# Optimization experiments

Hardware: AMD Instinct MI355X
Metric: run time of the kernel (lower is better)

## Reference

```python
import jax, jax.numpy as jnp
import numpy as np

EPS = 1e-5

def layernorm(x, w, b):
    m = jnp.mean(x, axis=-1, keepdims=True)
    v = jnp.var(x, axis=-1, keepdims=True)
    return (x - m) * jax.lax.rsqrt(v + EPS) * w + b

def setup_inputs() -> dict:
    key = jax.random.key(0)
    ks = jax.random.split(key, 20)
    B, N, D, H, C = 4, 2048, 512, 8, 3
    HID = int(D * 4.0 * (2.0 / 3.0))  # SwiGLU hidden = 1365
    g = lambda k, shape, s: (jax.random.normal(k, shape, jnp.float32) * s)
    return {
        "x": g(ks[0], (B, N, D), 1.0),
        "coords": jax.random.uniform(ks[1], (B, N, C), jnp.float32),
        "ln1_w": jnp.ones((D,), jnp.float32),
        "ln1_b": jnp.zeros((D,), jnp.float32),
        "ln2_w": jnp.ones((D,), jnp.float32),
        "ln2_b": jnp.zeros((D,), jnp.float32),
        "Wqkv": g(ks[2], (D, 3 * D), D ** -0.5),
        "bqkv": jnp.zeros((3 * D,), jnp.float32),
        "Wo": g(ks[3], (D, D), D ** -0.5),
        "bo": jnp.zeros((D,), jnp.float32),
        "Wc": g(ks[4], (C, H), 0.1),
        "bc": jnp.zeros((H,), jnp.float32),
        "W1": g(ks[5], (D, HID), D ** -0.5),
        "b1": jnp.zeros((HID,), jnp.float32),
        "W2": g(ks[6], (D, HID), D ** -0.5),
        "b2": jnp.zeros((HID,), jnp.float32),
        "W3": g(ks[7], (HID, D), HID ** -0.5),
        "b3": jnp.zeros((D,), jnp.float32),
    }

def reference(x, coords, ln1_w, ln1_b, ln2_w, ln2_b, Wqkv, bqkv, Wo, bo,
              Wc, bc, W1, b1, W2, b2, W3, b3):
    B, N, D = x.shape
    H = bc.shape[0]
    dh = D // H
    # --- coord-aware patch attention (pre-norm) ---
    h = layernorm(x, ln1_w, ln1_b)
    qkv = h @ Wqkv + bqkv                                # [B,N,3D]
    q, k, v = jnp.split(qkv, 3, axis=-1)
    to_heads = lambda t: t.reshape(B, N, H, dh).transpose(0, 2, 1, 3)  # [B,H,N,dh]
    q, k, v = to_heads(q), to_heads(k), to_heads(v)
    scores = jnp.einsum("bhnd,bhmd->bhnm", q, k) / np.sqrt(dh)
    rel = coords[:, :, None, :] - coords[:, None, :, :]  # [B,N,N,C]
    bias = jnp.einsum("bnmc,ch->bhnm", rel, Wc) + bc[None, :, None, None]
    attn = jax.nn.softmax(scores + bias, axis=-1)
    o = jnp.einsum("bhnm,bhmd->bhnd", attn, v)
    o = o.transpose(0, 2, 1, 3).reshape(B, N, D)
    x = x + (o @ Wo + bo)                                # residual 1
    # --- SwiGLU FFN (pre-norm) ---
    h2 = layernorm(x, ln2_w, ln2_b)
    ff = jax.nn.silu(h2 @ W1 + b1) * (h2 @ W2 + b2)
    x = x + (ff @ W3 + b3)                               # residual 2
    return x
```

## Files before the change

kernel.cpp:

```cpp
#include <hip/hip_runtime.h>
#include <hip/hip_bf16.h>
#include <math.h>

#define B_   4
#define N_   2048
#define D_   512
#define H_   8
#define DH_  64
#define C_   3
#define HID_ 1365
#define HIDP 1408
#define ROWS_ (B_*N_)
#define TD_  (3*D_)

typedef __attribute__((ext_vector_type(8))) short short8;
typedef __attribute__((ext_vector_type(4))) float floatx4;
typedef __attribute__((ext_vector_type(2))) unsigned uint2v;

#define MFMA16(a,b,c) __builtin_amdgcn_mfma_f32_16x16x32_bf16(a,b,c,0,0,0)

typedef __attribute__((address_space(3))) unsigned lds_u32;
typedef __attribute__((address_space(1))) unsigned glb_u32;

__device__ __forceinline__ short sh(float v){
  union { __hip_bfloat16 b; short s; } u;
  u.b = __float2bfloat16(v);
  return u.s;
}

__device__ __forceinline__ unsigned pk2(float a, float b){
  union { short s[2]; unsigned u; } z;
  z.s[0] = sh(a); z.s[1] = sh(b);
  return z.u;
}

__device__ __forceinline__ int swz(int col, int row){
  return (col & ~63) | (col & 7) | ((((col >> 3) & 7) ^ (row & 7)) << 3);
}

template<int ROWS, int PITCH>
__device__ __forceinline__ void stageG(short* __restrict__ lds,
    const short* __restrict__ g, int ldg, int t){
  const int LPR = PITCH/8;
  const int RPI = 64/LPR;
  const int PW  = (ROWS/RPI)/4;
  int lane = t & 63, w = t >> 6;
  #pragma unroll
  for (int i = 0; i < PW; ++i){
    int r0  = (w*PW + i)*RPI;
    int row = r0 + lane/LPR;
    const short* ga = g + (size_t)row*ldg + (lane % LPR)*8;
    short* la = lds + r0*PITCH;
    __builtin_amdgcn_global_load_lds((const glb_u32*)ga, (lds_u32*)la, 16, 0, 0);
  }
}

__device__ __forceinline__ short8 fragS(const short* __restrict__ lds, int pitch,
    int mbase, int lane, int kk){
  int row  = mbase + (lane & 15);
  int seg  = (kk >> 3) + (lane >> 4);
  int phys = seg ^ (row & 7);
  return *(const short8*)(lds + row*pitch + phys*8);
}

__global__ __launch_bounds__(256) void convT_all(
    const float* __restrict__ Wqkv, const float* __restrict__ Wo,
    const float* __restrict__ W1, const float* __restrict__ W2,
    const float* __restrict__ W3,
    short* __restrict__ Wtqkv, short* __restrict__ Wto,
    short* __restrict__ Wt1, short* __restrict__ Wt2, short* __restrict__ Wt3,
    const float* __restrict__ coords, const float* __restrict__ Wc,
    float* __restrict__ tv,
    const float* __restrict__ x, const float* __restrict__ ln1_w,
    const float* __restrict__ ln1_b, short* __restrict__ h){
  int id = blockIdx.x;
  int t = threadIdx.x;
  if (id >= 3392){
    int row = id - 3392;
    size_t base = (size_t)row * D_;
    float v0 = x[base + t];
    float v1 = x[base + t + 256];
    float s  = v0 + v1;
    float s2 = v0*v0 + v1*v1;
    #pragma unroll
    for (int off = 32; off >= 1; off >>= 1){
      s  += __shfl_xor(s,  off, 64);
      s2 += __shfl_xor(s2, off, 64);
    }
    __shared__ float red[8];
    int lane = t & 63, wv = t >> 6;
    if (lane == 0){ red[wv] = s; red[4+wv] = s2; }
    __syncthreads();
    float sum  = red[0]+red[1]+red[2]+red[3];
    float sum2 = red[4]+red[5]+red[6]+red[7];
    float mean = sum * (1.0f/D_);
    float var  = sum2 * (1.0f/D_) - mean*mean;
    float inv  = rsqrtf(fmaxf(var, 0.f) + 1e-5f);
    h[base + swz(t,     row)] = sh((v0-mean)*inv*ln1_w[t]     + ln1_b[t]);
    h[base + swz(t+256, row)] = sh((v1-mean)*inv*ln1_w[t+256] + ln1_b[t+256]);
    return;
  }
  if (id >= 3136){
    int idx = (id - 3136)*256 + t;
    int n = idx & (N_-1);
    int hh = (idx >> 11) & (H_-1);
    int b = idx >> 14;
    float s = 0.f;
    #pragma unroll
    for (int cc = 0; cc < C_; ++cc)
      s += coords[((size_t)(b*N_+n))*C_ + cc] * Wc[cc*H_ + hh];
    tv[idx] = s;
    return;
  }
  __shared__ float tile[32][33];
  const float* in; short* out; int K, NN, Kp, nx;
  if (id < 768)      { in=Wqkv; out=Wtqkv; K=512;  NN=1536; Kp=512;  nx=48; }
  else if (id < 1024){ in=Wo;   out=Wto;   K=512;  NN=512;  Kp=512;  nx=16; id-=768; }
  else if (id < 1728){ in=W1;   out=Wt1;   K=512;  NN=HID_; Kp=512;  nx=44; id-=1024; }
  else if (id < 2432){ in=W2;   out=Wt2;   K=512;  NN=HID_; Kp=512;  nx=44; id-=1728; }
  else               { in=W3;   out=Wt3;   K=HID_; NN=512;  Kp=HIDP; nx=16; id-=2432; }
  int nt0 = (id % nx)*32, kt0 = (id / nx)*32;
  int r = t >> 5, cc = t & 31;
  #pragma unroll
  for (int i=0;i<4;++i){
    int k = kt0 + i*8 + r, n = nt0 + cc;
    tile[i*8+r][cc] = (k<K && n<NN) ? in[(size_t)k*NN + n] : 0.f;
  }
  __syncthreads();
  #pragma unroll
  for (int i=0;i<4;++i){
    int n = nt0 + i*8 + r, k = kt0 + cc;
    out[(size_t)n*Kp + swz(k, n)] = sh(tile[cc][i*8+r]);
  }
}

__global__ __launch_bounds__(256) void ln_kernel(const float* __restrict__ x,
        const float* __restrict__ w, const float* __restrict__ b,
        short* __restrict__ out){
  int row = blockIdx.x;
  size_t base = (size_t)row * D_;
  int t = threadIdx.x;
  float v0 = x[base + t];
  float v1 = x[base + t + 256];
  float s  = v0 + v1;
  float s2 = v0*v0 + v1*v1;
  #pragma unroll
  for (int off = 32; off >= 1; off >>= 1){
    s  += __shfl_xor(s,  off, 64);
    s2 += __shfl_xor(s2, off, 64);
  }
  __shared__ float red[8];
  int lane = t & 63, wv = t >> 6;
  if (lane == 0){ red[wv] = s; red[4+wv] = s2; }
  __syncthreads();
  float sum  = red[0]+red[1]+red[2]+red[3];
  float sum2 = red[4]+red[5]+red[6]+red[7];
  float mean = sum * (1.0f/D_);
  float var  = sum2 * (1.0f/D_) - mean*mean;
  float inv  = rsqrtf(fmaxf(var, 0.f) + 1e-5f);
  out[base + swz(t,     row)] = sh((v0-mean)*inv*w[t]     + b[t]);
  out[base + swz(t+256, row)] = sh((v1-mean)*inv*w[t+256] + b[t+256]);
}

__global__ __launch_bounds__(256) void qkv_gemm(
    const short* __restrict__ A, const short* __restrict__ Bt,
    const float* __restrict__ bias,
    short* __restrict__ qb, short* __restrict__ kb, short* __restrict__ vbt){
  __shared__ short As[128*64];
  __shared__ short Bs[128*64];
  int t = threadIdx.x;
  int lane = t & 63, w = t >> 6;
  int wr = (w >> 1) * 64, wc = (w & 1) * 64;
  int col0 = blockIdx.x * 128, row0 = blockIdx.y * 128;
  floatx4 acc[4][4];
  #pragma unroll
  for (int mt=0;mt<4;++mt)
    #pragma unroll
    for (int nt=0;nt<4;++nt) acc[mt][nt] = (floatx4){0.f,0.f,0.f,0.f};
  for (int k0 = 0; k0 < D_; k0 += 64){
    __syncthreads();
    stageG<128,64>(As, A  + (size_t)row0*D_ + k0, D_, t);
    stageG<128,64>(Bs, Bt + (size_t)col0*D_ + k0, D_, t);
    __syncthreads();
    #pragma unroll
    for (int kk = 0; kk < 64; kk += 32){
      short8 af[4], bf[4];
      #pragma unroll
      for (int mt=0;mt<4;++mt) af[mt] = fragS(As, 64, wr+mt*16, lane, kk);
      #pragma unroll
      for (int nt=0;nt<4;++nt) bf[nt] = fragS(Bs, 64, wc+nt*16, lane, kk);
      #pragma unroll
      for (int mt=0;mt<4;++mt)
        #pragma unroll
        for (int nt=0;nt<4;++nt)
          acc[mt][nt] = MFMA16(af[mt], bf[nt], acc[mt][nt]);
    }
  }
  int quad = lane >> 4, c = lane & 15;
  #pragma unroll
  for (int mt=0;mt<4;++mt){
    #pragma unroll
    for (int nt=0;nt<4;++nt){
      #pragma unroll
      for (int r=0;r<4;++r){
        int row = row0 + wr + mt*16 + quad*4 + r;
        int col = col0 + wc + nt*16 + c;
        float v = acc[mt][nt][r] + bias[col];
        int bidx = row >> 11, n = row & (N_-1);
        int which = col >> 9, d = col & (D_-1), hh = d >> 6, hd = d & 63;
        short sv = sh(v);
        if (which == 0)
          qb[(((size_t)(bidx*H_ + hh))*N_ + n)*DH_ + swz(hd, n)] = sv;
        else if (which == 1)
          kb[(((size_t)(bidx*H_ + hh))*N_ + n)*DH_ + swz(hd, n)] = sv;
        else
          vbt[(((size_t)(bidx*H_ + hh))*DH_ + hd)*N_ + swz(n, hd)] = sv;
      }
    }
  }
}

__global__ __launch_bounds__(256) void gemm64(
    const short* __restrict__ A, int lda,
    const short* __restrict__ Bt, int Ktot,
    const float* __restrict__ bias,
    const float* __restrict__ resid, float* __restrict__ outF){
  __shared__ short As[128*64];
  __shared__ short Bs[64*64];
  int t = threadIdx.x, lane = t & 63, w = t >> 6;
  int wr = w * 32;
  int col0 = blockIdx.x * 64, row0 = blockIdx.y * 128;
  floatx4 acc[2][4];
  #pragma unroll
  for (int mt=0;mt<2;++mt)
    #pragma unroll
    for (int nt=0;nt<4;++nt) acc[mt][nt] = (floatx4){0.f,0.f,0.f,0.f};
  for (int k0 = 0; k0 < Ktot; k0 += 64){
    __syncthreads();
    stageG<128,64>(As, A  + (size_t)row0*lda + k0, lda, t);
    stageG<64,64> (Bs, Bt + (size_t)col0*Ktot + k0, Ktot, t);
    __syncthreads();
    #pragma unroll
    for (int kk = 0; kk < 64; kk += 32){
      short8 af[2], bf[4];
      #pragma unroll
      for (int mt=0;mt<2;++mt) af[mt] = fragS(As, 64, wr+mt*16, lane, kk);
      #pragma unroll
      for (int nt=0;nt<4;++nt) bf[nt] = fragS(Bs, 64, nt*16, lane, kk);
      #pragma unroll
      for (int mt=0;mt<2;++mt)
        #pragma unroll
        for (int nt=0;nt<4;++nt)
          acc[mt][nt] = MFMA16(af[mt], bf[nt], acc[mt][nt]);
    }
  }
  int quad = lane >> 4, c = lane & 15;
  #pragma unroll
  for (int mt=0;mt<2;++mt){
    #pragma unroll
    for (int nt=0;nt<4;++nt){
      #pragma unroll
      for (int r=0;r<4;++r){
        int row = row0 + wr + mt*16 + quad*4 + r;
        int col = col0 + nt*16 + c;
        size_t idx = (size_t)row*D_ + col;
        outF[idx] = acc[mt][nt][r] + bias[col] + resid[idx];
      }
    }
  }
}

__global__ __launch_bounds__(256) void gate_gemm(
    const short* __restrict__ A,
    const short* __restrict__ Bt1, const short* __restrict__ Bt2,
    const float* __restrict__ b1, const float* __restrict__ b2,
    short* __restrict__ ff){
  __shared__ short As[128*64];
  __shared__ short B1s[64*64];
  __shared__ short B2s[64*64];
  int t = threadIdx.x, lane = t & 63, w = t >> 6;
  int wr = (w >> 1) * 64, wc = (w & 1) * 32;
  int col0 = blockIdx.x * 64, row0 = blockIdx.y * 128;
  floatx4 a1[4][2], a2[4][2];
  #pragma unroll
  for (int mt=0;mt<4;++mt)
    #pragma unroll
    for (int nt=0;nt<2;++nt){
      a1[mt][nt] = (floatx4){0.f,0.f,0.f,0.f};
      a2[mt][nt] = (floatx4){0.f,0.f,0.f,0.f};
    }
  for (int k0 = 0; k0 < D_; k0 += 64){
    __syncthreads();
    stageG<128,64>(As, A + (size_t)row0*D_ + k0, D_, t);
    stageG<64,64>(B1s, Bt1 + (size_t)col0*D_ + k0, D_, t);
    stageG<64,64>(B2s, Bt2 + (size_t)col0*D_ + k0, D_, t);
    __syncthreads();
    #pragma unroll
    for (int kk = 0; kk < 64; kk += 32){
      short8 af[4], f1[2], f2[2];
      #pragma unroll
      for (int mt=0;mt<4;++mt) af[mt] = fragS(As, 64, wr+mt*16, lane, kk);
      #pragma unroll
      for (int nt=0;nt<2;++nt){
        f1[nt] = fragS(B1s, 64, wc+nt*16, lane, kk);
        f2[nt] = fragS(B2s, 64, wc+nt*16, lane, kk);
      }
      #pragma unroll
      for (int mt=0;mt<4;++mt)
        #pragma unroll
        for (int nt=0;nt<2;++nt){
          a1[mt][nt] = MFMA16(af[mt], f1[nt], a1[mt][nt]);
          a2[mt][nt] = MFMA16(af[mt], f2[nt], a2[mt][nt]);
        }
    }
  }
  int quad = lane >> 4, c = lane & 15;
  #pragma unroll
  for (int mt=0;mt<4;++mt){
    #pragma unroll
    for (int nt=0;nt<2;++nt){
      #pragma unroll
      for (int r=0;r<4;++r){
        int row = row0 + wr + mt*16 + quad*4 + r;
        int col = col0 + wc + nt*16 + c;
        float g1 = a1[mt][nt][r] + (col < HID_ ? b1[col] : 0.f);
        float g2 = a2[mt][nt][r] + (col < HID_ ? b2[col] : 0.f);
        float sig = 1.f / (1.f + __expf(-g1));
        ff[(size_t)row*HIDP + swz(col, row)] = sh(g1*sig*g2);
      }
    }
  }
}

#define EXP2SC 0.18033688011112042f
__global__ __launch_bounds__(256) void attn_mfma(
    const short* __restrict__ qb, const short* __restrict__ kbuf,
    const short* __restrict__ vbt, const float* __restrict__ tv,
    short* __restrict__ o){
  __shared__ short Ks2[2][128*64];
  __shared__ short Vt2[2][64*128];
  __shared__ __align__(16) float tsAll[2048];
  int qt = blockIdx.x, h = blockIdx.y, b = blockIdx.z;
  int bh = b*H_ + h;
  int t = threadIdx.x, lane = t & 63, w = t >> 6;
  int quad = lane >> 4, c = lane & 15;
  const short* Kbase = kbuf + (size_t)bh*N_*DH_;
  const short* Vbase = vbt  + (size_t)bh*DH_*N_;

  #pragma unroll
  for (int i = 0; i < 8; ++i)
    tsAll[i*256 + t] = tv[(size_t)bh*N_ + i*256 + t] * 1.44269504f;
  stageG<128,64>(Ks2[1], qb + ((size_t)bh*N_ + qt*128)*DH_, DH_, t);
  stageG<128,64>(Ks2[0], Kbase, DH_, t);
  stageG<64,128>(Vt2[0], Vbase, N_, t);
  __syncthreads();
  short8 qf[2][2];
  #pragma unroll
  for (int mt=0;mt<2;++mt)
    #pragma unroll
    for (int kh=0;kh<2;++kh)
      qf[mt][kh] = fragS(Ks2[1], 64, w*32 + mt*16, lane, kh*32);
  floatx4 O[2][4];
  float l_i[2] = {0.f, 0.f};
  #pragma unroll
  for (int mt=0;mt<2;++mt)
    #pragma unroll
    for (int nt=0;nt<4;++nt) O[mt][nt] = (floatx4){0.f,0.f,0.f,0.f};
  __syncthreads();

  for (int kt = 0; kt < N_/128; ++kt){
    int cur = kt & 1;
    if (kt + 1 < N_/128){
      stageG<128,64>(Ks2[cur^1], Kbase + (size_t)(kt+1)*128*DH_, DH_, t);
      stageG<64,128>(Vt2[cur^1], Vbase + (kt+1)*128, N_, t);
    }
    const short* Kc  = Ks2[cur];
    const short* Vc  = Vt2[cur];
    const float* tsc = tsAll + kt*128;
    #pragma unroll
    for (int kb4 = 0; kb4 < 4; ++kb4){
      floatx4 St[2][2];
      #pragma unroll
      for (int i=0;i<2;++i){
        St[i][0] = (floatx4){0.f,0.f,0.f,0.f};
        St[i][1] = (floatx4){0.f,0.f,0.f,0.f};
      }
      #pragma unroll
      for (int kh=0;kh<2;++kh){
        short8 kf0 = fragS(Kc, 64, kb4*32,      lane, kh*32);
        short8 kf1 = fragS(Kc, 64, kb4*32 + 16, lane, kh*32);
        #pragma unroll
        for (int mt=0;mt<2;++mt){
          St[0][mt] = MFMA16(kf0, qf[mt][kh], St[0][mt]);
          St[1][mt] = MFMA16(kf1, qf[mt][kh], St[1][mt]);
        }
      }
      floatx4 t0 = *(const floatx4*)&tsc[kb4*32 + quad*4];
      floatx4 t1 = *(const floatx4*)&tsc[kb4*32 + 16 + quad*4];
      short8 pbf[2];
      #pragma unroll
      for (int mt=0;mt<2;++mt){
        float p0[4], p1[4];
        #pragma unroll
        for (int r=0;r<4;++r){
          p0[r] = __builtin_amdgcn_exp2f(fmaf(St[0][mt][r], EXP2SC, -t0[r]));
          p1[r] = __builtin_amdgcn_exp2f(fmaf(St[1][mt][r], EXP2SC, -t1[r]));
        }
        l_i[mt] += (p0[0]+p0[1]) + (p0[2]+p0[3]) + (p1[0]+p1[1]) + (p1[2]+p1[3]);
        unsigned X0 = pk2(p0[0], p0[1]), X1 = pk2(p0[2], p0[3]);
        unsigned Y0 = pk2(p1[0], p1[1]), Y1 = pk2(p1[2], p1[3]);
        auto u0 = __builtin_amdgcn_permlane32_swap(X0, Y0, false, false);
        auto v0 = __builtin_amdgcn_permlane16_swap(u0[0], u0[1], false, false);
        auto u1 = __builtin_amdgcn_permlane32_swap(X1, Y1, false, false);
        auto v1 = __builtin_amdgcn_permlane16_swap(u1[0], u1[1], false, false);
        union { short8 s; unsigned uu[4]; } pb;
        pb.uu[0] = v0[0]; pb.uu[1] = v1[0]; pb.uu[2] = v0[1]; pb.uu[3] = v1[1];
        pbf[mt] = pb.s;
      }
      #pragma unroll
      for (int nt=0;nt<4;++nt){
        short8 vf = fragS(Vc, 128, nt*16, lane, kb4*32);
        #pragma unroll
        for (int mt=0;mt<2;++mt)
          O[mt][nt] = MFMA16(vf, pbf[mt], O[mt][nt]);
      }
    }
    __syncthreads();
  }
  #pragma unroll
  for (int mt=0;mt<2;++mt){
    float l = l_i[mt];
    l += __shfl_xor(l, 16, 64);
    l += __shfl_xor(l, 32, 64);
    float invl = 1.f / l;
    int qrow = qt*128 + w*32 + mt*16 + c;
    size_t rb = ((size_t)b*N_ + qrow)*(size_t)D_;
    #pragma unroll
    for (int nt=0;nt<4;++nt){
      int d0 = h*DH_ + nt*16 + quad*4;
      uint2v pv;
      pv.x = pk2(O[mt][nt][0]*invl, O[mt][nt][1]*invl);
      pv.y = pk2(O[mt][nt][2]*invl, O[mt][nt][3]*invl);
      *(uint2v*)(o + rb + swz(d0, qrow)) = pv;
    }
  }
}

extern "C" void kernel_launch(void* const* d_in, const int* in_sizes, int n_in,
                              void* d_out, int out_size, void* d_ws, size_t ws_size,
                              hipStream_t stream){
  const float* x      = (const float*)d_in[0];
  const float* coords = (const float*)d_in[1];
  const float* ln1_w  = (const float*)d_in[2];
  const float* ln1_b  = (const float*)d_in[3];
  const float* ln2_w  = (const float*)d_in[4];
  const float* ln2_b  = (const float*)d_in[5];
  const float* Wqkv   = (const float*)d_in[6];
  const float* bqkv   = (const float*)d_in[7];
  const float* Wo     = (const float*)d_in[8];
  const float* bo     = (const float*)d_in[9];
  const float* Wc     = (const float*)d_in[10];
  const float* W1     = (const float*)d_in[12];
  const float* b1     = (const float*)d_in[13];
  const float* W2     = (const float*)d_in[14];
  const float* b2     = (const float*)d_in[15];
  const float* W3     = (const float*)d_in[16];
  const float* b3     = (const float*)d_in[17];

  char* ws = (char*)d_ws;
  short* Wtqkv = (short*)(ws);
  short* Wto   = (short*)(ws + 1572864);
  short* Wt1   = (short*)(ws + 2097152);
  short* Wt2   = (short*)(ws + 3538944);
  short* Wt3   = (short*)(ws + 4980736);
  float* tv    = (float*)(ws + 6422528);
  short* h     = (short*)(ws + 6684672);
  short* qb    = (short*)(ws + 15073280);
  short* kb    = (short*)(ws + 23461888);
  short* vbt   = (short*)(ws + 31850496);
  short* o     = h;
  short* h2    = h;
  short* ff    = qb;
  float* x1    = (float*)d_out;

  convT_all<<<dim3(11584), dim3(256), 0, stream>>>(Wqkv, Wo, W1, W2, W3,
      Wtqkv, Wto, Wt1, Wt2, Wt3, coords, Wc, tv, x, ln1_w, ln1_b, h);
  qkv_gemm<<<dim3(12,64), dim3(256), 0, stream>>>(h, Wtqkv, bqkv, qb, kb, vbt);
  attn_mfma<<<dim3(16,8,4), dim3(256), 0, stream>>>(qb, kb, vbt, tv, o);
  gemm64<<<dim3(8,64), dim3(256), 0, stream>>>(o, 512, Wto, 512, bo, x, x1);
  ln_kernel<<<dim3(ROWS_), dim3(256), 0, stream>>>(x1, ln2_w, ln2_b, h2);
  gate_gemm<<<dim3(22,64), dim3(256), 0, stream>>>(h2, Wt1, Wt2, b1, b2, ff);
  gemm64<<<dim3(8,64), dim3(256), 0, stream>>>(ff, HIDP, Wt3, HIDP, b3, x1, x1);
}
```

Baseline: 310.8 us.

## Split attention key blocks across two wave groups with LDS reduction

Doubles the attention workgroup to 8 waves: four query groups times two key halves. Each half handles two of the four 32-key sub-blocks per tile, and partial outputs and row sums are combined through reused LDS before the final write. The log2e scaling of the coordinate bias moves into the precompute kernel, and tile loading uses vectorized loads. This aims to raise occupancy and latency hiding in attention, at the cost of an extra LDS reduction and higher per-block resource demand.

```diff
diff --git a/kernel.cpp b/kernel.cpp
--- a/kernel.cpp
+++ b/kernel.cpp
@@ -38,12 +38,12 @@
   return (col & ~63) | (col & 7) | ((((col >> 3) & 7) ^ (row & 7)) << 3);
 }
 
-template<int ROWS, int PITCH>
+template<int ROWS, int PITCH, int WAVES = 4>
 __device__ __forceinline__ void stageG(short* __restrict__ lds,
     const short* __restrict__ g, int ldg, int t){
   const int LPR = PITCH/8;
   const int RPI = 64/LPR;
-  const int PW  = (ROWS/RPI)/4;
+  const int PW  = (ROWS/RPI)/WAVES;
   int lane = t & 63, w = t >> 6;
   #pragma unroll
   for (int i = 0; i < PW; ++i){
@@ -109,7 +109,7 @@
     #pragma unroll
     for (int cc = 0; cc < C_; ++cc)
       s += coords[((size_t)(b*N_+n))*C_ + cc] * Wc[cc*H_ + hh];
-    tv[idx] = s;
+    tv[idx] = s * 1.44269504f;
     return;
   }
   __shared__ float tile[32][33];
@@ -333,7 +333,7 @@
 }
 
 #define EXP2SC 0.18033688011112042f
-__global__ __launch_bounds__(256) void attn_mfma(
+__global__ __launch_bounds__(512,4) void attn_mfma(
     const short* __restrict__ qb, const short* __restrict__ kbuf,
     const short* __restrict__ vbt, const float* __restrict__ tv,
     short* __restrict__ o){
@@ -343,23 +343,22 @@
   int qt = blockIdx.x, h = blockIdx.y, b = blockIdx.z;
   int bh = b*H_ + h;
   int t = threadIdx.x, lane = t & 63, w = t >> 6;
+  int qg = w & 3, kg = w >> 2;
   int quad = lane >> 4, c = lane & 15;
   const short* Kbase = kbuf + (size_t)bh*N_*DH_;
   const short* Vbase = vbt  + (size_t)bh*DH_*N_;
 
-  #pragma unroll
-  for (int i = 0; i < 8; ++i)
-    tsAll[i*256 + t] = tv[(size_t)bh*N_ + i*256 + t] * 1.44269504f;
-  stageG<128,64>(Ks2[1], qb + ((size_t)bh*N_ + qt*128)*DH_, DH_, t);
-  stageG<128,64>(Ks2[0], Kbase, DH_, t);
-  stageG<64,128>(Vt2[0], Vbase, N_, t);
+  *(floatx4*)&tsAll[t*4] = *(const floatx4*)&tv[(size_t)bh*N_ + t*4];
+  stageG<128,64,8>(Ks2[1], qb + ((size_t)bh*N_ + qt*128)*DH_, DH_, t);
+  stageG<128,64,8>(Ks2[0], Kbase, DH_, t);
+  stageG<64,128,8>(Vt2[0], Vbase, N_, t);
   __syncthreads();
   short8 qf[2][2];
   #pragma unroll
   for (int mt=0;mt<2;++mt)
     #pragma unroll
     for (int kh=0;kh<2;++kh)
-      qf[mt][kh] = fragS(Ks2[1], 64, w*32 + mt*16, lane, kh*32);
+      qf[mt][kh] = fragS(Ks2[1], 64, qg*32 + mt*16, lane, kh*32);
   floatx4 O[2][4];
   float l_i[2] = {0.f, 0.f};
   #pragma unroll
@@ -371,14 +370,15 @@
   for (int kt = 0; kt < N_/128; ++kt){
     int cur = kt & 1;
     if (kt + 1 < N_/128){
-      stageG<128,64>(Ks2[cur^1], Kbase + (size_t)(kt+1)*128*DH_, DH_, t);
-      stageG<64,128>(Vt2[cur^1], Vbase + (kt+1)*128, N_, t);
+      stageG<128,64,8>(Ks2[cur^1], Kbase + (size_t)(kt+1)*128*DH_, DH_, t);
+      stageG<64,128,8>(Vt2[cur^1], Vbase + (kt+1)*128, N_, t);
     }
     const short* Kc  = Ks2[cur];
     const short* Vc  = Vt2[cur];
     const float* tsc = tsAll + kt*128;
     #pragma unroll
-    for (int kb4 = 0; kb4 < 4; ++kb4){
+    for (int kb = 0; kb < 2; ++kb){
+      int kb4 = kg*2 + kb;
       floatx4 St[2][2];
       #pragma unroll
       for (int i=0;i<2;++i){
@@ -427,21 +427,42 @@
     }
     __syncthreads();
   }
-  #pragma unroll
-  for (int mt=0;mt<2;++mt){
-    float l = l_i[mt];
-    l += __shfl_xor(l, 16, 64);
-    l += __shfl_xor(l, 32, 64);
-    float invl = 1.f / l;
-    int qrow = qt*128 + w*32 + mt*16 + c;
-    size_t rb = ((size_t)b*N_ + qrow)*(size_t)D_;
-    #pragma unroll
-    for (int nt=0;nt<4;++nt){
-      int d0 = h*DH_ + nt*16 + quad*4;
-      uint2v pv;
-      pv.x = pk2(O[mt][nt][0]*invl, O[mt][nt][1]*invl);
-      pv.y = pk2(O[mt][nt][2]*invl, O[mt][nt][3]*invl);
-      *(uint2v*)(o + rb + swz(d0, qrow)) = pv;
+  float* Om = (float*)Vt2;
+  float* Lm = (float*)Ks2;
+  if (kg == 1){
+    #pragma unroll
+    for (int mt=0;mt<2;++mt){
+      #pragma unroll
+      for (int nt=0;nt<4;++nt)
+        *(floatx4*)&Om[(((qg*2+mt)*4+nt)*64 + lane)*4] = O[mt][nt];
+      Lm[(qg*2+mt)*64 + lane] = l_i[mt];
+    }
+  }
+  __syncthreads();
+  if (kg == 0){
+    #pragma unroll
+    for (int mt=0;mt<2;++mt){
+      l_i[mt] += Lm[(qg*2+mt)*64 + lane];
+      #pragma unroll
+      for (int nt=0;nt<4;++nt)
+        O[mt][nt] += *(const floatx4*)&Om[(((qg*2+mt)*4+nt)*64 + lane)*4];
+    }
+    #pragma unroll
+    for (int mt=0;mt<2;++mt){
+      float l = l_i[mt];
+      l += __shfl_xor(l, 16, 64);
+      l += __shfl_xor(l, 32, 64);
+      float invl = 1.f / l;
+      int qrow = qt*128 + qg*32 + mt*16 + c;
+      size_t rb = ((size_t)b*N_ + qrow)*(size_t)D_;
+      #pragma unroll
+      for (int nt=0;nt<4;++nt){
+        int d0 = h*DH_ + nt*16 + quad*4;
+        uint2v pv;
+        pv.x = pk2(O[mt][nt][0]*invl, O[mt][nt][1]*invl);
+        pv.y = pk2(O[mt][nt][2]*invl, O[mt][nt][3]*invl);
+        *(uint2v*)(o + rb + swz(d0, qrow)) = pv;
+      }
     }
   }
 }
@@ -486,7 +507,7 @@
   convT_all<<<dim3(11584), dim3(256), 0, stream>>>(Wqkv, Wo, W1, W2, W3,
       Wtqkv, Wto, Wt1, Wt2, Wt3, coords, Wc, tv, x, ln1_w, ln1_b, h);
   qkv_gemm<<<dim3(12,64), dim3(256), 0, stream>>>(h, Wtqkv, bqkv, qb, kb, vbt);
-  attn_mfma<<<dim3(16,8,4), dim3(256), 0, stream>>>(qb, kb, vbt, tv, o);
+  attn_mfma<<<dim3(16,8,4), dim3(512), 0, stream>>>(qb, kb, vbt, tv, o);
   gemm64<<<dim3(8,64), dim3(256), 0, stream>>>(o, 512, Wto, 512, bo, x, x1);
   ln_kernel<<<dim3(ROWS_), dim3(256), 0, stream>>>(x1, ln2_w, ln2_b, h2);
   gate_gemm<<<dim3(22,64), dim3(256), 0, stream>>>(h2, Wt1, Wt2, b1, b2, ff);
```

After: 321.4 us. 3.4% more time.

## Double-buffer gemm64 LDS tiles and vectorize layernorm and bias-table loads

Applied to the files above, without the earlier changes.

gemm64 now keeps two LDS buffers for A and B. The next K-tile is prefetched with global_load_lds while MFMAs run on the current tile, leaving one barrier per iteration and hiding load latency. The two layernorm kernels read x, w and b as float2 and write packed bf16 pairs. The log2e scaling of the coordinate bias table moves into the precompute kernel, so attention loads that table with 16-byte vector loads. The cost is double the LDS in gemm64, which may lower occupancy.

```diff
diff --git a/kernel.cpp b/kernel.cpp
--- a/kernel.cpp
+++ b/kernel.cpp
@@ -38,12 +38,12 @@
   return (col & ~63) | (col & 7) | ((((col >> 3) & 7) ^ (row & 7)) << 3);
 }
 
-template<int ROWS, int PITCH>
+template<int ROWS, int PITCH, int WAVES = 4>
 __device__ __forceinline__ void stageG(short* __restrict__ lds,
     const short* __restrict__ g, int ldg, int t){
   const int LPR = PITCH/8;
   const int RPI = 64/LPR;
-  const int PW  = (ROWS/RPI)/4;
+  const int PW  = (ROWS/RPI)/WAVES;
   int lane = t & 63, w = t >> 6;
   #pragma unroll
   for (int i = 0; i < PW; ++i){
@@ -78,10 +78,9 @@
   if (id >= 3392){
     int row = id - 3392;
     size_t base = (size_t)row * D_;
-    float v0 = x[base + t];
-    float v1 = x[base + t + 256];
-    float s  = v0 + v1;
-    float s2 = v0*v0 + v1*v1;
+    float2 u = *(const float2*)&x[base + 2*t];
+    float s  = u.x + u.y;
+    float s2 = u.x*u.x + u.y*u.y;
     #pragma unroll
     for (int off = 32; off >= 1; off >>= 1){
       s  += __shfl_xor(s,  off, 64);
@@ -96,8 +95,10 @@
     float mean = sum * (1.0f/D_);
     float var  = sum2 * (1.0f/D_) - mean*mean;
     float inv  = rsqrtf(fmaxf(var, 0.f) + 1e-5f);
-    h[base + swz(t,     row)] = sh((v0-mean)*inv*ln1_w[t]     + ln1_b[t]);
-    h[base + swz(t+256, row)] = sh((v1-mean)*inv*ln1_w[t+256] + ln1_b[t+256]);
+    float2 wv2 = *(const float2*)&ln1_w[2*t];
+    float2 bv2 = *(const float2*)&ln1_b[2*t];
+    *(unsigned*)(h + base + swz(2*t, row)) =
+        pk2((u.x-mean)*inv*wv2.x + bv2.x, (u.y-mean)*inv*wv2.y + bv2.y);
     return;
   }
   if (id >= 3136){
@@ -109,7 +110,7 @@
     #pragma unroll
     for (int cc = 0; cc < C_; ++cc)
       s += coords[((size_t)(b*N_+n))*C_ + cc] * Wc[cc*H_ + hh];
-    tv[idx] = s;
+    tv[idx] = s * 1.44269504f;
     return;
   }
   __shared__ float tile[32][33];
@@ -140,10 +141,9 @@
   int row = blockIdx.x;
   size_t base = (size_t)row * D_;
   int t = threadIdx.x;
-  float v0 = x[base + t];
-  float v1 = x[base + t + 256];
-  float s  = v0 + v1;
-  float s2 = v0*v0 + v1*v1;
+  float2 u = *(const float2*)&x[base + 2*t];
+  float s  = u.x + u.y;
+  float s2 = u.x*u.x + u.y*u.y;
   #pragma unroll
   for (int off = 32; off >= 1; off >>= 1){
     s  += __shfl_xor(s,  off, 64);
@@ -158,8 +158,10 @@
   float mean = sum * (1.0f/D_);
   float var  = sum2 * (1.0f/D_) - mean*mean;
   float inv  = rsqrtf(fmaxf(var, 0.f) + 1e-5f);
-  out[base + swz(t,     row)] = sh((v0-mean)*inv*w[t]     + b[t]);
-  out[base + swz(t+256, row)] = sh((v1-mean)*inv*w[t+256] + b[t+256]);
+  float2 wv2 = *(const float2*)&w[2*t];
+  float2 bv2 = *(const float2*)&b[2*t];
+  *(unsigned*)(out + base + swz(2*t, row)) =
+      pk2((u.x-mean)*inv*wv2.x + bv2.x, (u.y-mean)*inv*wv2.y + bv2.y);
 }
 
 __global__ __launch_bounds__(256) void qkv_gemm(
@@ -225,8 +227,8 @@
     const short* __restrict__ Bt, int Ktot,
     const float* __restrict__ bias,
     const float* __restrict__ resid, float* __restrict__ outF){
-  __shared__ short As[128*64];
-  __shared__ short Bs[64*64];
+  __shared__ short As[2][128*64];
+  __shared__ short Bs[2][64*64];
   int t = threadIdx.x, lane = t & 63, w = t >> 6;
   int wr = w * 32;
   int col0 = blockIdx.x * 64, row0 = blockIdx.y * 128;
@@ -235,18 +237,23 @@
   for (int mt=0;mt<2;++mt)
     #pragma unroll
     for (int nt=0;nt<4;++nt) acc[mt][nt] = (floatx4){0.f,0.f,0.f,0.f};
-  for (int k0 = 0; k0 < Ktot; k0 += 64){
-    __syncthreads();
-    stageG<128,64>(As, A  + (size_t)row0*lda + k0, lda, t);
-    stageG<64,64> (Bs, Bt + (size_t)col0*Ktot + k0, Ktot, t);
-    __syncthreads();
+  stageG<128,64>(As[0], A  + (size_t)row0*lda, lda, t);
+  stageG<64,64> (Bs[0], Bt + (size_t)col0*Ktot, Ktot, t);
+  const int NT = Ktot >> 6;
+  for (int ti = 0; ti < NT; ++ti){
+    int cur = ti & 1;
+    __syncthreads();
+    if (ti + 1 < NT){
+      stageG<128,64>(As[cur^1], A  + (size_t)row0*lda + (ti+1)*64, lda, t);
+      stageG<64,64> (Bs[cur^1], Bt + (size_t)col0*Ktot + (ti+1)*64, Ktot, t);
+    }
     #pragma unroll
     for (int kk = 0; kk < 64; kk += 32){
       short8 af[2], bf[4];
       #pragma unroll
-      for (int mt=0;mt<2;++mt) af[mt] = fragS(As, 64, wr+mt*16, lane, kk);
-      #pragma unroll
-      for (int nt=0;nt<4;++nt) bf[nt] = fragS(Bs, 64, nt*16, lane, kk);
+      for (int mt=0;mt<2;++mt) af[mt] = fragS(As[cur], 64, wr+mt*16, lane, kk);
+      #pragma unroll
+      for (int nt=0;nt<4;++nt) bf[nt] = fragS(Bs[cur], 64, nt*16, lane, kk);
       #pragma unroll
       for (int mt=0;mt<2;++mt)
         #pragma unroll
@@ -348,8 +355,8 @@
   const short* Vbase = vbt  + (size_t)bh*DH_*N_;
 
   #pragma unroll
-  for (int i = 0; i < 8; ++i)
-    tsAll[i*256 + t] = tv[(size_t)bh*N_ + i*256 + t] * 1.44269504f;
+  for (int i = 0; i < 2; ++i)
+    *(floatx4*)&tsAll[t*8 + i*4] = *(const floatx4*)&tv[(size_t)bh*N_ + t*8 + i*4];
   stageG<128,64>(Ks2[1], qb + ((size_t)bh*N_ + qt*128)*DH_, DH_, t);
   stageG<128,64>(Ks2[0], Kbase, DH_, t);
   stageG<64,128>(Vt2[0], Vbase, N_, t);
```

After: 313.6 us. Within noise of the previous version (+0.9%).
